# Kernel tuning notes

Measured on AMD Instinct MI355X. Metric: run time of the kernel, lower is better.

The kernel has to match this reference:

```python
import jax, jax.numpy as jnp
import numpy as np

IMAGE_C = 1
IMAGE_W = 28
PIXELS_PER_ROW = IMAGE_W * IMAGE_C  # 28

B, T, E = 16, IMAGE_W * IMAGE_W * IMAGE_C, 512  # T = 784
H = 8
D = E // H  # head_dim = 64


def get_2d_causal_bias(T):
    idx = jnp.arange(T)
    i = idx // PIXELS_PER_ROW          # row index
    j = (idx % PIXELS_PER_ROW) // IMAGE_C  # col index
    c = idx % IMAGE_C                  # channel index
    q_i, k_i = i[:, None], i[None, :]
    q_j, k_j = j[:, None], j[None, :]
    q_c, k_c = c[:, None], c[None, :]
    allowed = (k_i < q_i) | ((k_i == q_i) & (k_j < q_j)) | (
        (k_i == q_i) & (k_j == q_j) & (k_c <= q_c))
    bias = jnp.where(allowed, 0.0, -jnp.inf).astype(jnp.float32)
    return bias[None, None]  # [1, 1, T, T]


def setup_inputs() -> dict:
    key = jax.random.key(0)
    ks = jax.random.split(key, 5)
    s = 1.0 / np.sqrt(E)
    return {
        "x": jax.random.normal(ks[0], (B, T, E), dtype=jnp.float32),
        "Wq": jax.random.normal(ks[1], (E, E), dtype=jnp.float32) * s,
        "bq": jnp.zeros((E,), dtype=jnp.float32),
        "Wk": jax.random.normal(ks[2], (E, E), dtype=jnp.float32) * s,
        "bk": jnp.zeros((E,), dtype=jnp.float32),
        "Wv": jax.random.normal(ks[3], (E, E), dtype=jnp.float32) * s,
        "bv": jnp.zeros((E,), dtype=jnp.float32),
        "Wo": jax.random.normal(ks[4], (E, E), dtype=jnp.float32) * s,
        "bo": jnp.zeros((E,), dtype=jnp.float32),
    }


def reference(x, Wq, bq, Wk, bk, Wv, bv, Wo, bo):
    Bx, Tx, Ex = x.shape
    # projections (torch Linear: y = x @ W.T + b; here W stored as [E, E] used directly)
    Q = (x @ Wq + bq).reshape(Bx, Tx, H, D).transpose(0, 2, 1, 3)  # [B,H,T,D]
    K = (x @ Wk + bk).reshape(Bx, Tx, H, D).transpose(0, 2, 1, 3)
    V = (x @ Wv + bv).reshape(Bx, Tx, H, D).transpose(0, 2, 1, 3)
    scores = jnp.einsum("bhqd,bhkd->bhqk", Q, K) / jnp.sqrt(jnp.float32(D))
    scores = scores + get_2d_causal_bias(Tx)
    attn = jax.nn.softmax(scores, axis=-1)
    ctx = jnp.einsum("bhqk,bhkd->bhqd", attn, V)
    ctx = ctx.transpose(0, 2, 1, 3).reshape(Bx, Tx, Ex)
    return ctx @ Wo + bo
```

## Files before the change

kernel.cpp:

```cpp
#include <hip/hip_runtime.h>
#include <hip/hip_bf16.h>

#define BB    16
#define TT    784
#define TPK   832
#define TPQ   896
#define EE    512
#define HH    8
#define DD    64
#define BT    (BB*TT)

typedef short short8 __attribute__((ext_vector_type(8)));
typedef short short4v __attribute__((ext_vector_type(4)));
typedef float floatx4 __attribute__((ext_vector_type(4)));

__device__ __forceinline__ short f2bf(float f) {
    unsigned u = __builtin_bit_cast(unsigned, f);
    u += 0x7FFFu + ((u >> 16) & 1u);
    return (short)(u >> 16);
}

__global__ void prep_kernel(const float* __restrict__ x, short* __restrict__ xb,
                            const float* __restrict__ Wq, const float* __restrict__ Wk,
                            const float* __restrict__ Wv, short* __restrict__ wqkvt,
                            const float* __restrict__ Wo, short* __restrict__ wot,
                            short* __restrict__ Qb, short* __restrict__ Kb, short* __restrict__ Vt)
{
    __shared__ short t[64][65];
    int b = blockIdx.x;
    if (b < 3136) {
        int i = (b * 256 + threadIdx.x) * 8;
        float4 a = *(const float4*)(x + i);
        float4 c = *(const float4*)(x + i + 4);
        short8 o;
        o[0] = f2bf(a.x); o[1] = f2bf(a.y); o[2] = f2bf(a.z); o[3] = f2bf(a.w);
        o[4] = f2bf(c.x); o[5] = f2bf(c.y); o[6] = f2bf(c.z); o[7] = f2bf(c.w);
        *(short8*)(xb + i) = o;
    } else if (b < 3392) {
        const float* W; short* out; int n0, k0;
        if (b < 3328) {
            int tt = b - 3136;
            n0 = (tt % 24) * 64; k0 = (tt / 24) * 64;
            W = (n0 < 512) ? Wq : (n0 < 1024 ? Wk : Wv);
            out = wqkvt;
        } else {
            int tt = b - 3328;
            n0 = (tt % 8) * 64; k0 = (tt / 8) * 64;
            W = Wo; out = wot;
        }
        int nn0 = n0 & 511;
        for (int i = threadIdx.x; i < 4096; i += 256) {
            int r = i >> 6, c = i & 63;
            t[r][c] = f2bf(W[(k0 + r) * 512 + nn0 + c]);
        }
        __syncthreads();
        for (int i = threadIdx.x; i < 4096; i += 256) {
            int nr = i >> 6, kc = i & 63;
            out[(n0 + nr) * 512 + k0 + kc] = t[kc][nr];
        }
    } else {
        int c = (b - 3392) * 256 + threadIdx.x;
        short8 z = (short8){0,0,0,0,0,0,0,0};
        if (c < 114688) {
            int bh = c / 896, j = c - bh * 896;
            *(short8*)&Qb[(bh * TPQ + TT) * 64 + j * 8] = z;
        } else if (c < 163840) {
            int c2 = c - 114688;
            int bh = c2 / 384, j = c2 - bh * 384;
            *(short8*)&Kb[(bh * TPK + TT) * 64 + j * 8] = z;
        } else {
            int c3 = c - 163840;
            int bh = c3 / 384, j = c3 - bh * 384;
            int d = j / 6, m = j - d * 6;
            *(short8*)&Vt[(bh * 64 + d) * TPK + TT + m * 8] = z;
        }
    }
}

__global__ __launch_bounds__(256, 4) void gemm_qkv_kernel(
    const short* __restrict__ A, const short* __restrict__ Bt,
    const float* __restrict__ bq, const float* __restrict__ bk, const float* __restrict__ bv,
    short* __restrict__ Qb, short* __restrict__ Kb, short* __restrict__ Vt)
{
    __shared__ __align__(16) short smem[16640];
    short* As0 = smem;
    short* Bs0 = smem + 8192;

    const int m0 = blockIdx.x * 128, n0 = blockIdx.y * 128;
    const int tid = threadIdx.x;
    const int lane = tid & 63, w = tid >> 6;
    const int wr = w >> 1, wc = w & 1;
    const int l16 = lane & 15, quad = lane >> 4;

    const int srow = w * 32 + (lane >> 2);
    const int scol = (lane & 3) * 8;
    const short* Ag = A  + (size_t)(m0 + srow) * 512 + scol;
    const short* Bg = Bt + (size_t)(n0 + srow) * 512 + scol;
    const int soff = srow * 32 + scol;

    short8 areg[2], breg[2];
    auto load_regs = [&](int it) {
        int ko = it * 32;
        areg[0] = *(const short8*)(Ag + ko);
        areg[1] = *(const short8*)(Ag + ko + 16 * 512);
        breg[0] = *(const short8*)(Bg + ko);
        breg[1] = *(const short8*)(Bg + ko + 16 * 512);
    };
    auto store_regs = [&](int b) {
        *(short8*)&As0[b * 4096 + soff]            = areg[0];
        *(short8*)&As0[b * 4096 + soff + 16 * 32]  = areg[1];
        *(short8*)&Bs0[b * 4096 + soff]            = breg[0];
        *(short8*)&Bs0[b * 4096 + soff + 16 * 32]  = breg[1];
    };

    floatx4 acc[4][4];
    #pragma unroll
    for (int i = 0; i < 4; i++)
        #pragma unroll
        for (int j = 0; j < 4; j++)
            acc[i][j] = (floatx4){0.f, 0.f, 0.f, 0.f};

    load_regs(0);
    store_regs(0);

    for (int it = 0; it < 16; it++) {
        if (it < 15) load_regs(it + 1);
        __syncthreads();
        const short* as = As0 + (it & 1) * 4096;
        const short* bs = Bs0 + (it & 1) * 4096;
        short8 af[4], bf[4];
        #pragma unroll
        for (int i = 0; i < 4; i++) {
            af[i] = *(const short8*)&as[(wr * 64 + i * 16 + l16) * 32 + quad * 8];
            bf[i] = *(const short8*)&bs[(wc * 64 + i * 16 + l16) * 32 + quad * 8];
        }
        #pragma unroll
        for (int mi = 0; mi < 4; mi++)
            #pragma unroll
            for (int ni = 0; ni < 4; ni++)
                acc[mi][ni] = __builtin_amdgcn_mfma_f32_16x16x32_bf16(af[mi], bf[ni], acc[mi][ni], 0, 0, 0);
        if (it < 15) store_regs((it + 1) & 1);
    }

    const int sel = n0 >> 9;
    if (sel == 2) {
        #pragma unroll
        for (int mi = 0; mi < 4; mi++) {
            int m = m0 + wr * 64 + mi * 16 + quad * 4;
            int bb = m / TT, t = m - bb * TT;
            #pragma unroll
            for (int ni = 0; ni < 4; ni++) {
                int nn = (n0 + wc * 64 + ni * 16 + l16) & 511;
                int hh = nn >> 6, dd = nn & 63;
                float b = bv[nn];
                short4v pv;
                #pragma unroll
                for (int r = 0; r < 4; r++) pv[r] = f2bf(acc[mi][ni][r] + b);
                *(short4v*)&Vt[((size_t)(bb * HH + hh) * 64 + dd) * TPK + t] = pv;
            }
        }
    } else {
        __syncthreads();
        short* Ct = smem;
        const float* bias = (sel == 0) ? bq : bk;
        #pragma unroll
        for (int mi = 0; mi < 4; mi++) {
            #pragma unroll
            for (int ni = 0; ni < 4; ni++) {
                int nl = wc * 64 + ni * 16 + l16;
                int nn = (n0 + nl) & 511;
                float b = bias[nn];
                #pragma unroll
                for (int r = 0; r < 4; r++) {
                    float v = acc[mi][ni][r] + b;
                    if (sel == 0) v *= 0.125f;
                    Ct[(wr * 64 + mi * 16 + quad * 4 + r) * 130 + nl] = f2bf(v);
                }
            }
        }
        __syncthreads();
        short* dst = (sel == 0) ? Qb : Kb;
        const int tp = (sel == 0) ? TPQ : TPK;
        int nl = lane * 2;
        int nn = (n0 + nl) & 511;
        int hh = nn >> 6, dd = nn & 63;
        #pragma unroll 4
        for (int rr = 0; rr < 32; rr++) {
            int ml = w * 32 + rr;
            int m = m0 + ml;
            int bb = m / TT, t = m - bb * TT;
            unsigned pv = *(const unsigned*)&Ct[ml * 130 + nl];
            *(unsigned*)&dst[((bb * HH + hh) * tp + t) * 64 + dd] = pv;
        }
    }
}

#define LK 72
__global__ __launch_bounds__(256, 3) void attn_kernel(
    const short* __restrict__ Qb, const short* __restrict__ Kb, const short* __restrict__ Vt,
    short* __restrict__ ctx)
{
    const int g = blockIdx.x;
    const int low = g & 7, rest = g >> 3;
    const int qt = 12 - (rest >> 4);
    const int bh = ((rest & 15) << 3) | low;
    const int bb = bh >> 3, hh = bh & 7;
    const int tid = threadIdx.x;
    const int lane = tid & 63, w = tid >> 6;
    const int l16 = lane & 15, quad = lane >> 4;

    __shared__ short Ks[2][64 * LK];
    __shared__ short Vs[2][64 * LK];
    __shared__ short Ps[64 * LK];

    const int srow = tid >> 3;
    const int sc8 = (tid & 7) * 8;
    const short* Kbase = Kb + (size_t)(bh * TPK) * 64;
    const short* Vbase = Vt + (size_t)(bh * 64) * TPK;

    short8 kreg[2], vreg[2];
    auto load_tile = [&](int kt) {
        #pragma unroll
        for (int p = 0; p < 2; p++) {
            int row = srow + p * 32;
            kreg[p] = *(const short8*)(Kbase + (kt * 64 + row) * 64 + sc8);
            vreg[p] = *(const short8*)(Vbase + row * TPK + kt * 64 + sc8);
        }
    };
    auto store_tile = [&](int b) {
        #pragma unroll
        for (int p = 0; p < 2; p++) {
            int row = srow + p * 32;
            *(short8*)&Ks[b][row * LK + sc8] = kreg[p];
            *(short8*)&Vs[b][row * LK + sc8] = vreg[p];
        }
    };

    const short* Qrow = Qb + (size_t)(bh * TPQ + qt * 64 + w * 16 + l16) * 64;
    short8 qa0 = *(const short8*)(Qrow + quad * 8);
    short8 qa1 = *(const short8*)(Qrow + 32 + quad * 8);

    floatx4 accO[4];
    floatx4 accL = (floatx4){0.f, 0.f, 0.f, 0.f};
    #pragma unroll
    for (int dt = 0; dt < 4; dt++) accO[dt] = (floatx4){0.f, 0.f, 0.f, 0.f};

    short8 ones8;
    #pragma unroll
    for (int j = 0; j < 8; j++) ones8[j] = (short)0x3F80;

    const int pswz  = (quad >> 1) * 16;
    const int prswz = ((l16 >> 3) & 1) * 16;
    short* Pw = &Ps[(w * 16 + quad * 4) * LK];

    load_tile(0);
    store_tile(0);

    for (int kt = 0; kt <= qt; kt++) {
        const int cb = kt & 1;
        const bool diag = (kt == qt);
        if (kt < qt) load_tile(kt + 1);
        __syncthreads();

        float p[4][4];
        #pragma unroll
        for (int ni = 0; ni < 4; ni++) {
            if (diag && ni > w) {
                #pragma unroll
                for (int r = 0; r < 4; r++) p[ni][r] = 0.f;
                continue;
            }
            short8 kb0 = *(short8*)&Ks[cb][(ni * 16 + l16) * LK + quad * 8];
            short8 kb1 = *(short8*)&Ks[cb][(ni * 16 + l16) * LK + 32 + quad * 8];
            floatx4 z = (floatx4){0.f, 0.f, 0.f, 0.f};
            z = __builtin_amdgcn_mfma_f32_16x16x32_bf16(qa0, kb0, z, 0, 0, 0);
            z = __builtin_amdgcn_mfma_f32_16x16x32_bf16(qa1, kb1, z, 0, 0, 0);
            if (diag && ni == w) {
                #pragma unroll
                for (int r = 0; r < 4; r++)
                    if (l16 > quad * 4 + r) z[r] = -1e30f;
            }
            #pragma unroll
            for (int r = 0; r < 4; r++) p[ni][r] = __expf(z[r]);
        }

        #pragma unroll
        for (int ni = 0; ni < 4; ni++) {
            int col = (ni * 16 + l16) ^ pswz;
            #pragma unroll
            for (int r = 0; r < 4; r++)
                Pw[r * LK + col] = (short)(__builtin_bit_cast(unsigned, p[ni][r]) >> 16);
        }

        #pragma unroll
        for (int kk = 0; kk < 2; kk++) {
            if (diag && (kk * 32 > w * 16 + 15)) continue;
            short8 pa = *(short8*)&Ps[(w * 16 + l16) * LK + ((kk * 32 + quad * 8) ^ prswz)];
            accL = __builtin_amdgcn_mfma_f32_16x16x32_bf16(pa, ones8, accL, 0, 0, 0);
            #pragma unroll
            for (int dt = 0; dt < 4; dt++) {
                short8 vb = *(short8*)&Vs[cb][(dt * 16 + l16) * LK + kk * 32 + quad * 8];
                accO[dt] = __builtin_amdgcn_mfma_f32_16x16x32_bf16(pa, vb, accO[dt], 0, 0, 0);
            }
        }

        if (kt < qt) store_tile((kt + 1) & 1);
    }

    float inv_l[4];
    #pragma unroll
    for (int r = 0; r < 4; r++) inv_l[r] = 1.f / accL[r];
    #pragma unroll
    for (int dt = 0; dt < 4; dt++)
        #pragma unroll
        for (int r = 0; r < 4; r++) {
            int qg = qt * 64 + w * 16 + quad * 4 + r;
            if (qg < TT)
                ctx[(size_t)(bb * TT + qg) * 512 + hh * 64 + dt * 16 + l16] = f2bf(accO[dt][r] * inv_l[r]);
        }
}

__global__ __launch_bounds__(256, 4) void gemm_out_kernel(
    const short* __restrict__ A, const short* __restrict__ Bt,
    const float* __restrict__ bo, float* __restrict__ out)
{
    __shared__ __align__(16) short smem[16384];
    short* As0 = smem;
    short* Bs0 = smem + 8192;

    const int m0 = blockIdx.x * 128, n0 = blockIdx.y * 128;
    const int tid = threadIdx.x;
    const int lane = tid & 63, w = tid >> 6;
    const int wr = w >> 1, wc = w & 1;
    const int l16 = lane & 15, quad = lane >> 4;

    const int srow = w * 32 + (lane >> 2);
    const int scol = (lane & 3) * 8;
    const short* Ag = A  + (size_t)(m0 + srow) * 512 + scol;
    const short* Bg = Bt + (size_t)(n0 + srow) * 512 + scol;
    const int soff = srow * 32 + scol;

    short8 areg[2], breg[2];
    auto load_regs = [&](int it) {
        int ko = it * 32;
        areg[0] = *(const short8*)(Ag + ko);
        areg[1] = *(const short8*)(Ag + ko + 16 * 512);
        breg[0] = *(const short8*)(Bg + ko);
        breg[1] = *(const short8*)(Bg + ko + 16 * 512);
    };
    auto store_regs = [&](int b) {
        *(short8*)&As0[b * 4096 + soff]            = areg[0];
        *(short8*)&As0[b * 4096 + soff + 16 * 32]  = areg[1];
        *(short8*)&Bs0[b * 4096 + soff]            = breg[0];
        *(short8*)&Bs0[b * 4096 + soff + 16 * 32]  = breg[1];
    };

    floatx4 acc[4][4];
    #pragma unroll
    for (int i = 0; i < 4; i++)
        #pragma unroll
        for (int j = 0; j < 4; j++)
            acc[i][j] = (floatx4){0.f, 0.f, 0.f, 0.f};

    load_regs(0);
    store_regs(0);

    for (int it = 0; it < 16; it++) {
        if (it < 15) load_regs(it + 1);
        __syncthreads();
        const short* as = As0 + (it & 1) * 4096;
        const short* bs = Bs0 + (it & 1) * 4096;
        short8 af[4], bf[4];
        #pragma unroll
        for (int i = 0; i < 4; i++) {
            af[i] = *(const short8*)&as[(wr * 64 + i * 16 + l16) * 32 + quad * 8];
            bf[i] = *(const short8*)&bs[(wc * 64 + i * 16 + l16) * 32 + quad * 8];
        }
        #pragma unroll
        for (int mi = 0; mi < 4; mi++)
            #pragma unroll
            for (int ni = 0; ni < 4; ni++)
                acc[mi][ni] = __builtin_amdgcn_mfma_f32_16x16x32_bf16(af[mi], bf[ni], acc[mi][ni], 0, 0, 0);
        if (it < 15) store_regs((it + 1) & 1);
    }

    #pragma unroll
    for (int mi = 0; mi < 4; mi++) {
        #pragma unroll
        for (int ni = 0; ni < 4; ni++) {
            int n = n0 + wc * 64 + ni * 16 + l16;
            float bias = bo[n];
            #pragma unroll
            for (int r = 0; r < 4; r++) {
                int m = m0 + wr * 64 + mi * 16 + quad * 4 + r;
                out[(size_t)m * 512 + n] = acc[mi][ni][r] + bias;
            }
        }
    }
}

extern "C" void kernel_launch(void* const* d_in, const int* in_sizes, int n_in,
                              void* d_out, int out_size, void* d_ws, size_t ws_size,
                              hipStream_t stream) {
    const float* x  = (const float*)d_in[0];
    const float* Wq = (const float*)d_in[1];
    const float* bq = (const float*)d_in[2];
    const float* Wk = (const float*)d_in[3];
    const float* bk = (const float*)d_in[4];
    const float* Wv = (const float*)d_in[5];
    const float* bv = (const float*)d_in[6];
    const float* Wo = (const float*)d_in[7];
    const float* bo = (const float*)d_in[8];
    float* out = (float*)d_out;

    char* ws = (char*)d_ws;
    size_t off = 0;
    auto alloc = [&](size_t bytes) -> void* {
        void* p = ws + off;
        off += (bytes + 255) & ~(size_t)255;
        return p;
    };
    short* xb    = (short*)alloc((size_t)BT * EE * 2);
    short* wqkvt = (short*)alloc((size_t)1536 * 512 * 2);
    short* wot   = (short*)alloc((size_t)512 * 512 * 2);
    short* Qb    = (short*)alloc((size_t)BB * HH * TPQ * DD * 2);
    short* Kb    = (short*)alloc((size_t)BB * HH * TPK * DD * 2);
    short* Vtb   = (short*)alloc((size_t)BB * HH * DD * TPK * 2);
    short* ctxb  = (short*)alloc((size_t)BT * EE * 2);

    prep_kernel<<<4224, 256, 0, stream>>>(x, xb, Wq, Wk, Wv, wqkvt, Wo, wot, Qb, Kb, Vtb);
    gemm_qkv_kernel<<<dim3(98, 12), 256, 0, stream>>>(xb, wqkvt, bq, bk, bv, Qb, Kb, Vtb);
    attn_kernel<<<1664, 256, 0, stream>>>(Qb, Kb, Vtb, ctxb);
    gemm_out_kernel<<<dim3(98, 4), 256, 0, stream>>>(ctxb, wot, bo, out);
}
```

Baseline: 166.0 us.

## Rewrite attention kernel with 32x32 MFMA, transposed scores in registers, split-K waves

The attention kernel now computes transposed score tiles (K·Q^T) with 32x32x16 bf16 MFMAs. This lets the exp'd probabilities feed directly as the B operand of the PV MFMA, with no round-trip through shared memory. Waves are split into a 2x2 grid of query halves and key halves, and the key-half partial sums are reduced through LDS at the end. K/V shared tiles use XOR swizzling instead of padding, row sums are accumulated in scalar registers instead of via a ones-MFMA, and bf16 packing uses v_cvt_pk_bf16_f32. The cost is an extra LDS reduction, a barrier, and higher register pressure from the 16-wide accumulators.

```diff
diff --git a/kernel.cpp b/kernel.cpp
--- a/kernel.cpp
+++ b/kernel.cpp
@@ -13,11 +13,19 @@
 typedef short short8 __attribute__((ext_vector_type(8)));
 typedef short short4v __attribute__((ext_vector_type(4)));
 typedef float floatx4 __attribute__((ext_vector_type(4)));
+typedef float floatx16 __attribute__((ext_vector_type(16)));
+typedef unsigned uint4v __attribute__((ext_vector_type(4)));
 
 __device__ __forceinline__ short f2bf(float f) {
     unsigned u = __builtin_bit_cast(unsigned, f);
     u += 0x7FFFu + ((u >> 16) & 1u);
     return (short)(u >> 16);
+}
+
+__device__ __forceinline__ unsigned cvtpk_bf16(float lo, float hi) {
+    unsigned r;
+    asm("v_cvt_pk_bf16_f32 %0, %1, %2" : "=v"(r) : "v"(lo), "v"(hi));
+    return r;
 }
 
 __global__ void prep_kernel(const float* __restrict__ x, short* __restrict__ xb,
@@ -195,7 +203,6 @@
     }
 }
 
-#define LK 72
 __global__ __launch_bounds__(256, 3) void attn_kernel(
     const short* __restrict__ Qb, const short* __restrict__ Kb, const short* __restrict__ Vt,
     short* __restrict__ ctx)
@@ -207,117 +214,141 @@
     const int bb = bh >> 3, hh = bh & 7;
     const int tid = threadIdx.x;
     const int lane = tid & 63, w = tid >> 6;
-    const int l16 = lane & 15, quad = lane >> 4;
-
-    __shared__ short Ks[2][64 * LK];
-    __shared__ short Vs[2][64 * LK];
-    __shared__ short Ps[64 * LK];
-
-    const int srow = tid >> 3;
-    const int sc8 = (tid & 7) * 8;
+    const int wq = w >> 1, wk = w & 1;
+    const int l32 = lane & 31, hi = lane >> 5;
+    const int r7 = l32 & 7;
+
+    __shared__ __align__(16) short Ks[2][4096];
+    __shared__ __align__(16) short Vs[2][4096];
+
     const short* Kbase = Kb + (size_t)(bh * TPK) * 64;
     const short* Vbase = Vt + (size_t)(bh * 64) * TPK;
 
+    const int srow = tid >> 3;
+    const int sc8  = tid & 7;
+    const int scol = sc8 * 8;
+    const int ksw  = (sc8 ^ (srow & 7)) * 8;
+    const int vg0  = (sc8 >> 1) * 2;
+    const int vsw0 = ((vg0       ^ (srow & 7)) * 8) + (sc8 & 1) * 4;
+    const int vsw1 = (((vg0 + 1) ^ (srow & 7)) * 8) + (sc8 & 1) * 4;
+
     short8 kreg[2], vreg[2];
     auto load_tile = [&](int kt) {
         #pragma unroll
         for (int p = 0; p < 2; p++) {
             int row = srow + p * 32;
-            kreg[p] = *(const short8*)(Kbase + (kt * 64 + row) * 64 + sc8);
-            vreg[p] = *(const short8*)(Vbase + row * TPK + kt * 64 + sc8);
+            kreg[p] = *(const short8*)(Kbase + (kt * 64 + row) * 64 + scol);
+            vreg[p] = *(const short8*)(Vbase + row * TPK + kt * 64 + scol);
         }
     };
     auto store_tile = [&](int b) {
         #pragma unroll
         for (int p = 0; p < 2; p++) {
-            int row = srow + p * 32;
-            *(short8*)&Ks[b][row * LK + sc8] = kreg[p];
-            *(short8*)&Vs[b][row * LK + sc8] = vreg[p];
-        }
-    };
-
-    const short* Qrow = Qb + (size_t)(bh * TPQ + qt * 64 + w * 16 + l16) * 64;
-    short8 qa0 = *(const short8*)(Qrow + quad * 8);
-    short8 qa1 = *(const short8*)(Qrow + 32 + quad * 8);
-
-    floatx4 accO[4];
-    floatx4 accL = (floatx4){0.f, 0.f, 0.f, 0.f};
+            int ro = (srow + p * 32) * 64;
+            *(short8*)&Ks[b][ro + ksw] = kreg[p];
+            short4v v0, v1;
+            #pragma unroll
+            for (int i = 0; i < 4; i++) { v0[i] = vreg[p][i]; v1[i] = vreg[p][i + 4]; }
+            *(short4v*)&Vs[b][ro + vsw0] = v0;
+            *(short4v*)&Vs[b][ro + vsw1] = v1;
+        }
+    };
+
+    const int q_lo = qt * 64 + wq * 32;
+    const int qg = q_lo + l32;
+    const bool wreal = (q_lo < TT);
+    const short* Qrow = Qb + (size_t)(bh * TPQ + qg) * 64;
+    short8 qf[4];
     #pragma unroll
-    for (int dt = 0; dt < 4; dt++) accO[dt] = (floatx4){0.f, 0.f, 0.f, 0.f};
-
-    short8 ones8;
+    for (int d = 0; d < 4; d++) qf[d] = *(const short8*)(Qrow + d * 16 + hi * 8);
+
+    floatx16 accO[2];
     #pragma unroll
-    for (int j = 0; j < 8; j++) ones8[j] = (short)0x3F80;
-
-    const int pswz  = (quad >> 1) * 16;
-    const int prswz = ((l16 >> 3) & 1) * 16;
-    short* Pw = &Ps[(w * 16 + quad * 4) * LK];
+    for (int dt = 0; dt < 2; dt++)
+        #pragma unroll
+        for (int i = 0; i < 16; i++) accO[dt][i] = 0.f;
+    float accL = 0.f;
 
     load_tile(0);
     store_tile(0);
 
     for (int kt = 0; kt <= qt; kt++) {
         const int cb = kt & 1;
-        const bool diag = (kt == qt);
         if (kt < qt) load_tile(kt + 1);
         __syncthreads();
-
-        float p[4][4];
-        #pragma unroll
-        for (int ni = 0; ni < 4; ni++) {
-            if (diag && ni > w) {
-                #pragma unroll
-                for (int r = 0; r < 4; r++) p[ni][r] = 0.f;
-                continue;
-            }
-            short8 kb0 = *(short8*)&Ks[cb][(ni * 16 + l16) * LK + quad * 8];
-            short8 kb1 = *(short8*)&Ks[cb][(ni * 16 + l16) * LK + 32 + quad * 8];
-            floatx4 z = (floatx4){0.f, 0.f, 0.f, 0.f};
-            z = __builtin_amdgcn_mfma_f32_16x16x32_bf16(qa0, kb0, z, 0, 0, 0);
-            z = __builtin_amdgcn_mfma_f32_16x16x32_bf16(qa1, kb1, z, 0, 0, 0);
-            if (diag && ni == w) {
-                #pragma unroll
-                for (int r = 0; r < 4; r++)
-                    if (l16 > quad * 4 + r) z[r] = -1e30f;
-            }
-            #pragma unroll
-            for (int r = 0; r < 4; r++) p[ni][r] = __expf(z[r]);
-        }
-
-        #pragma unroll
-        for (int ni = 0; ni < 4; ni++) {
-            int col = (ni * 16 + l16) ^ pswz;
-            #pragma unroll
-            for (int r = 0; r < 4; r++)
-                Pw[r * LK + col] = (short)(__builtin_bit_cast(unsigned, p[ni][r]) >> 16);
-        }
-
-        #pragma unroll
-        for (int kk = 0; kk < 2; kk++) {
-            if (diag && (kk * 32 > w * 16 + 15)) continue;
-            short8 pa = *(short8*)&Ps[(w * 16 + l16) * LK + ((kk * 32 + quad * 8) ^ prswz)];
-            accL = __builtin_amdgcn_mfma_f32_16x16x32_bf16(pa, ones8, accL, 0, 0, 0);
-            #pragma unroll
-            for (int dt = 0; dt < 4; dt++) {
-                short8 vb = *(short8*)&Vs[cb][(dt * 16 + l16) * LK + kk * 32 + quad * 8];
-                accO[dt] = __builtin_amdgcn_mfma_f32_16x16x32_bf16(pa, vb, accO[dt], 0, 0, 0);
-            }
-        }
-
+        const int kbase = kt * 64 + wk * 32;
+        if (wreal && kbase <= q_lo + 31) {
+            floatx16 z;
+            #pragma unroll
+            for (int i = 0; i < 16; i++) z[i] = 0.f;
+            #pragma unroll
+            for (int d = 0; d < 4; d++) {
+                short8 kf = *(const short8*)&Ks[cb][(wk * 32 + l32) * 64 + (((d * 2 + hi) ^ r7) * 8)];
+                z = __builtin_amdgcn_mfma_f32_32x32x16_bf16(kf, qf[d], z, 0, 0, 0);
+            }
+            float p[16];
+            #pragma unroll
+            for (int r = 0; r < 16; r++) p[r] = __expf(z[r]);
+            if (kbase + 31 > q_lo) {
+                #pragma unroll
+                for (int r = 0; r < 16; r++) {
+                    int keyg = kbase + (r & 3) + 8 * (r >> 2) + 4 * hi;
+                    if (keyg > qg) p[r] = 0.f;
+                }
+            }
+            #pragma unroll
+            for (int r = 0; r < 16; r++) accL += p[r];
+            #pragma unroll
+            for (int s = 0; s < 2; s++) {
+                uint4v pw;
+                #pragma unroll
+                for (int jj = 0; jj < 4; jj++)
+                    pw[jj] = cvtpk_bf16(p[8 * s + 2 * jj], p[8 * s + 2 * jj + 1]);
+                short8 pb = __builtin_bit_cast(short8, pw);
+                #pragma unroll
+                for (int dt = 0; dt < 2; dt++) {
+                    short8 vf = *(const short8*)&Vs[cb][(dt * 32 + l32) * 64 + (((wk * 4 + s * 2 + hi) ^ r7) * 8)];
+                    accO[dt] = __builtin_amdgcn_mfma_f32_32x32x16_bf16(vf, pb, accO[dt], 0, 0, 0);
+                }
+            }
+        }
         if (kt < qt) store_tile((kt + 1) & 1);
     }
 
-    float inv_l[4];
-    #pragma unroll
-    for (int r = 0; r < 4; r++) inv_l[r] = 1.f / accL[r];
-    #pragma unroll
-    for (int dt = 0; dt < 4; dt++)
-        #pragma unroll
-        for (int r = 0; r < 4; r++) {
-            int qg = qt * 64 + w * 16 + quad * 4 + r;
-            if (qg < TT)
-                ctx[(size_t)(bb * TT + qg) * 512 + hh * 64 + dt * 16 + l16] = f2bf(accO[dt][r] * inv_l[r]);
-        }
+    __syncthreads();
+    float* rbuf  = (float*)&Ks[0][0];
+    float* rbufL = (float*)&Vs[0][0];
+    if (wk == 1) {
+        #pragma unroll
+        for (int dt = 0; dt < 2; dt++)
+            #pragma unroll
+            for (int r = 0; r < 16; r++)
+                rbuf[((wq * 2 + dt) * 16 + r) * 64 + lane] = accO[dt][r];
+        rbufL[wq * 64 + lane] = accL;
+    }
+    __syncthreads();
+    if (wk == 0) {
+        #pragma unroll
+        for (int dt = 0; dt < 2; dt++)
+            #pragma unroll
+            for (int r = 0; r < 16; r++)
+                accO[dt][r] += rbuf[((wq * 2 + dt) * 16 + r) * 64 + lane];
+        accL += rbufL[wq * 64 + lane];
+        float Lt = accL + __shfl_xor(accL, 32, 64);
+        if (wreal && qg < TT) {
+            float inv = 1.f / Lt;
+            short* crow = ctx + (size_t)(bb * TT + qg) * 512 + hh * 64;
+            #pragma unroll
+            for (int dt = 0; dt < 2; dt++)
+                #pragma unroll
+                for (int g4 = 0; g4 < 4; g4++) {
+                    short4v pv;
+                    #pragma unroll
+                    for (int r4 = 0; r4 < 4; r4++) pv[r4] = f2bf(accO[dt][g4 * 4 + r4] * inv);
+                    *(short4v*)&crow[dt * 32 + g4 * 8 + 4 * hi] = pv;
+                }
+        }
+    }
 }
 
 __global__ __launch_bounds__(256, 4) void gemm_out_kernel(
```

New measurement: 163.3 us. About the same (-1.6%).
